# Kernel tuning notes

Hardware: AMD Instinct MI355X
Metric: run time of the kernel (lower is better)

Reference implementation:

```python
import jax, jax.numpy as jnp
import numpy as np

N = 100000   # nodes
E = 800000   # edges
G = 64       # graphs in batch
H_LSTM = 256


def setup_inputs() -> dict:
    key = jax.random.key(0)
    ks = jax.random.split(key, 24)

    def rn(k, shape, scale=0.05):
        return jax.random.normal(k, shape, dtype=jnp.float32) * scale

    inp = {
        "x": jax.random.normal(ks[0], (N, 32), dtype=jnp.float32),
        "edge_index": jax.random.randint(ks[1], (2, E), 0, N, dtype=jnp.int64),
        "batch_idx": jnp.sort(jax.random.randint(ks[2], (N,), 0, G, dtype=jnp.int64)),
        # GCN layer weights (in_dim x out_dim) + bias
        "W1": rn(ks[3], (32, 128)),   "b1": jnp.zeros((128,), jnp.float32),
        "W2": rn(ks[4], (128, 256)),  "b2": jnp.zeros((256,), jnp.float32),
        "W3": rn(ks[5], (256, 512)),  "b3": jnp.zeros((512,), jnp.float32),
        # LSTM layer 0: input 512 -> hidden 256, gates order (i,f,g,o)
        "Wih0": rn(ks[6], (4 * H_LSTM, 512)), "Whh0": rn(ks[7], (4 * H_LSTM, H_LSTM)),
        "bih0": jnp.zeros((4 * H_LSTM,), jnp.float32), "bhh0": jnp.zeros((4 * H_LSTM,), jnp.float32),
        # LSTM layer 1: input 256 -> hidden 256
        "Wih1": rn(ks[8], (4 * H_LSTM, H_LSTM)), "Whh1": rn(ks[9], (4 * H_LSTM, H_LSTM)),
        "bih1": jnp.zeros((4 * H_LSTM,), jnp.float32), "bhh1": jnp.zeros((4 * H_LSTM,), jnp.float32),
        # output projection 256 -> 512
        "Wp": rn(ks[10], (512, H_LSTM)), "bp": jnp.zeros((512,), jnp.float32),
    }
    return inp


def _lstm_cell(xt, Wih, Whh, bih, bhh):
    B = xt.shape[0]
    H = Whh.shape[1]
    h0 = jnp.zeros((B, H), xt.dtype)
    c0 = jnp.zeros((B, H), xt.dtype)
    gates = xt @ Wih.T + h0 @ Whh.T + bih + bhh  # [B, 4H]
    i = jax.nn.sigmoid(gates[:, 0 * H:1 * H])
    f = jax.nn.sigmoid(gates[:, 1 * H:2 * H])
    g = jnp.tanh(gates[:, 2 * H:3 * H])
    o = jax.nn.sigmoid(gates[:, 3 * H:4 * H])
    c = f * c0 + i * g
    return o * jnp.tanh(c)


def reference(x, edge_index, batch_idx, W1, b1, W2, b2, W3, b3,
              Wih0, Whh0, bih0, bhh0, Wih1, Whh1, bih1, bhh1, Wp, bp):
    src, dst = edge_index[0], edge_index[1]
    # symmetric GCN normalization with self-loops (PyG GCNConv default)
    deg = jax.ops.segment_sum(jnp.ones((E,), x.dtype), dst, num_segments=N) + 1.0
    dinv = jax.lax.rsqrt(deg)
    edge_norm = (dinv[src] * dinv[dst])[:, None]
    self_norm = (dinv * dinv)[:, None]

    def gcn(h, W, b):
        h = h @ W                                            # transform first (smaller gather)
        msg = h[src] * edge_norm                             # [E, out]
        agg = jax.ops.segment_sum(msg, dst, num_segments=N)  # scatter-add to targets
        agg = agg + h * self_norm                            # self-loop contribution
        return jax.nn.relu(agg + b)

    h = gcn(x, W1, b1)
    h = gcn(h, W2, b2)
    h = gcn(h, W3, b3)  # [N, 512]

    # global mean pool per graph
    counts = jax.ops.segment_sum(jnp.ones((N,), h.dtype), batch_idx, num_segments=G)
    pooled = jax.ops.segment_sum(h, batch_idx, num_segments=G) / jnp.maximum(counts, 1.0)[:, None]

    # 2-layer LSTM over seq_len=1 (zero initial state)
    h1 = _lstm_cell(pooled, Wih0, Whh0, bih0, bhh0)
    h2 = _lstm_cell(h1, Wih1, Whh1, bih1, bhh1)
    return h2 @ Wp.T + bp  # [G, 512]
```

## Files before the change

kernel.cpp:

```cpp
#include <hip/hip_runtime.h>
#include <math.h>
#include <type_traits>


__device__ __forceinline__ float bf2f(unsigned short u) {
    union { unsigned int i; float f; } v; v.i = ((unsigned int)u) << 16; return v.f;
}
__device__ __forceinline__ unsigned short f2bf(float f) {
    union { float f_; unsigned int i; } v; v.f_ = f;
    unsigned int x = v.i;
    return (unsigned short)((x + 0x7fffu + ((x >> 16) & 1u)) >> 16);
}
__device__ __forceinline__ float sigm(float x) { return 1.f / (1.f + expf(-x)); }

typedef __attribute__((ext_vector_type(8))) short short8;
typedef __attribute__((ext_vector_type(16))) float f32x16;

__device__ __forceinline__ void nt_store8(unsigned short* p, ushort4 o) {
    unsigned long long ob;
    __builtin_memcpy(&ob, &o, 8);
    __builtin_nontemporal_store(ob, (unsigned long long*)p);
}


__global__ void k_init(int* __restrict__ indeg, int* __restrict__ cursor,
                       int* __restrict__ gstart, int* __restrict__ gend,
                       float* __restrict__ pooled, int N) {
    int i = blockIdx.x * 256 + threadIdx.x;
    if (i < N) indeg[i] = 0;
    else if (i < 2 * N) cursor[i - N] = 0;
    else if (i < 2 * N + 64) gstart[i - 2 * N] = 0;
    else if (i < 2 * N + 128) gend[i - 2 * N - 64] = 0;
    else if (i < 2 * N + 128 + 64 * 512) pooled[i - 2 * N - 128] = 0.f;
}


template <int K, int NC>
__device__ __forceinline__ void prep_elem(const float* __restrict__ W,
                                          unsigned short* __restrict__ Wf, int idx) {
    constexpr int S = K / 16;
    int lane = idx & 63;
    int ts = idx >> 6;
    int s = ts % S, t = ts / S;
    int n = t * 32 + (lane & 31);
    int kb = s * 16 + (lane >> 5) * 8;
    short8 o;
    #pragma unroll
    for (int j = 0; j < 8; ++j) o[j] = (short)f2bf(W[(size_t)(kb + j) * NC + n]);
    *(short8*)(Wf + (size_t)idx * 8) = o;
}

__global__ void k_count(const int* __restrict__ dst, int* __restrict__ indeg, int E,
                        const float* __restrict__ W1, unsigned short* __restrict__ Wf1,
                        const float* __restrict__ W2, unsigned short* __restrict__ Wf2,
                        const float* __restrict__ W3, unsigned short* __restrict__ Wf3) {
    constexpr int P1 = 32 * 128 / 8, P2 = 128 * 256 / 8, P3 = 256 * 512 / 8;
    int i = blockIdx.x * 256 + threadIdx.x;
    if (i < E) atomicAdd(&indeg[dst[i]], 1);
    if (i < P1) prep_elem<32, 128>(W1, Wf1, i);
    else if (i < P1 + P2) prep_elem<128, 256>(W2, Wf2, i - P1);
    else if (i < P1 + P2 + P3) prep_elem<256, 512>(W3, Wf3, i - P1 - P2);
}


__global__ __launch_bounds__(1024) void k_scan1(const int* __restrict__ in, int* __restrict__ out,
                                                int* __restrict__ bsum, float* __restrict__ dinv,
                                                const float* __restrict__ x,
                                                unsigned short* __restrict__ xs,
                                                int N) {
    __shared__ int sd[1024];
    __shared__ float sdv[1024];
    int tid = threadIdx.x;
    int i = blockIdx.x * 1024 + tid;
    int v = (i < N) ? in[i] : 0;
    float dv = rsqrtf((float)v + 1.0f);
    if (i < N) dinv[i] = dv;
    sdv[tid] = dv;
    sd[tid] = v;
    __syncthreads();
    for (int s = 1; s < 1024; s <<= 1) {
        int t = (tid >= s) ? sd[tid - s] : 0;
        __syncthreads();
        sd[tid] += t;
        __syncthreads();
    }
    if (i < N) out[i] = sd[tid] - v;
    if (tid == 1023) bsum[blockIdx.x] = sd[1023];
    int base = blockIdx.x * 1024;
    const float4* x4 = (const float4*)x;
    ushort4* xs4 = (ushort4*)xs;
    #pragma unroll
    for (int rep = 0; rep < 8; ++rep) {
        int j = rep * 1024 + tid;
        int node = base + (j >> 3);
        if (node < N) {
            float4 t = x4[(size_t)base * 8 + j];
            float s = sdv[j >> 3];
            ushort4 o;
            o.x = f2bf(t.x * s); o.y = f2bf(t.y * s);
            o.z = f2bf(t.z * s); o.w = f2bf(t.w * s);
            xs4[(size_t)base * 8 + j] = o;
        }
    }
}

__global__ __launch_bounds__(256) void k_scan2(int* __restrict__ bsum, int nb) {
    __shared__ int sd[256];
    int tid = threadIdx.x;
    int v = (tid < nb) ? bsum[tid] : 0;
    sd[tid] = v;
    __syncthreads();
    for (int s = 1; s < 256; s <<= 1) {
        int t = (tid >= s) ? sd[tid - s] : 0;
        __syncthreads();
        sd[tid] += t;
        __syncthreads();
    }
    if (tid < nb) bsum[tid] = sd[tid] - v;
    if (tid == 0) bsum[nb] = sd[255];
}

__global__ __launch_bounds__(1024) void k_scan3(int* __restrict__ off, const int* __restrict__ bsum,
                                                const int* __restrict__ batch,
                                                int* __restrict__ gstart, int* __restrict__ gend,
                                                int N, int nb) {
    int i = blockIdx.x * 1024 + threadIdx.x;
    if (i < N) {
        off[i] += bsum[i >> 10];
        int g = batch[i];
        if (i == 0 || batch[i - 1] != g) gstart[g] = i;
        if (i == N - 1 || batch[i + 1] != g) gend[g] = i + 1;
    } else if (i == N) {
        off[N] = bsum[nb];
    }
}

__global__ void k_fill(const int* __restrict__ src, const int* __restrict__ dst,
                       const int* __restrict__ off, int* __restrict__ cursor,
                       int* __restrict__ csrc, int E) {
    int i = blockIdx.x * 256 + threadIdx.x;
    if (i >= E) return;
    int d = dst[i];
    int p = off[d] + atomicAdd(&cursor[d], 1);
    csrc[p] = src[i];
}


__global__ __launch_bounds__(256) void k_aggL1(
        const unsigned short* __restrict__ Hin, const float* __restrict__ dinv,
        const int* __restrict__ off, const int* __restrict__ csrc,
        unsigned short* __restrict__ out, int N) {
    constexpr int F = 32;
    int wv = __builtin_amdgcn_readfirstlane(
        (int)((blockIdx.x * 256u + threadIdx.x) >> 6));
    if (wv >= N) return;
    int lane = threadIdx.x & 63;
    int grp = lane >> 3;
    int cl = (lane & 7) * 4;
    int s0 = off[wv], s1 = off[wv + 1];
    int L = s1 - s0;
    float corr = 1.0f - (float)(((L + 7) & ~7) - L);
    float dn = dinv[wv];
    float acc[4] = {0.f, 0.f, 0.f, 0.f};
    for (int e = s0; e < s1; e += 8) {
        int ee = e + grp;
        int ix = csrc[ee];
        int idx = (ee < s1) ? ix : wv;
        ushort4 v = *(const ushort4*)(Hin + (size_t)idx * F + cl);
        acc[0] += bf2f(v.x); acc[1] += bf2f(v.y);
        acc[2] += bf2f(v.z); acc[3] += bf2f(v.w);
    }
    #pragma unroll
    for (int msk = 8; msk <= 32; msk <<= 1) {
        acc[0] += __shfl_xor(acc[0], msk, 64);
        acc[1] += __shfl_xor(acc[1], msk, 64);
        acc[2] += __shfl_xor(acc[2], msk, 64);
        acc[3] += __shfl_xor(acc[3], msk, 64);
    }
    if (grp == 0) {
        ushort4 sv = *(const ushort4*)(Hin + (size_t)wv * F + cl);
        ushort4 o;
        o.x = f2bf((acc[0] + corr * bf2f(sv.x)) * dn);
        o.y = f2bf((acc[1] + corr * bf2f(sv.y)) * dn);
        o.z = f2bf((acc[2] + corr * bf2f(sv.z)) * dn);
        o.w = f2bf((acc[3] + corr * bf2f(sv.w)) * dn);
        nt_store8(out + (size_t)wv * F + cl, o);
    }
}

__global__ __launch_bounds__(256) void k_aggL2(
        const unsigned short* __restrict__ Hin, const float* __restrict__ dinv,
        const int* __restrict__ off, const int* __restrict__ csrc,
        unsigned short* __restrict__ out, int N) {
    constexpr int F = 128;
    int wv = __builtin_amdgcn_readfirstlane(
        (int)((blockIdx.x * 256u + threadIdx.x) >> 6));
    if (wv >= N) return;
    int lane = threadIdx.x & 63;
    int half = lane >> 5;
    int fb = (lane & 31) * 4;
    int s0 = off[wv], s1 = off[wv + 1];
    int L = s1 - s0;
    float corrTot = 1.0f - (float)(((L + 15) & ~15) - L);
    float acc[4] = {0.f, 0.f, 0.f, 0.f};

    for (int e = s0; e < s1; e += 16) {
        int idx[8];
        #pragma unroll
        for (int j = 0; j < 8; ++j) {
            int ee = e + j * 2 + half;
            int ix = csrc[ee];
            idx[j] = (ee < s1) ? ix : wv;
        }
        ushort4 d0[8];
        #pragma unroll
        for (int j = 0; j < 8; ++j)
            d0[j] = *(const ushort4*)(Hin + (size_t)idx[j] * F + fb);
        #pragma unroll
        for (int j = 0; j < 8; ++j) {
            acc[0] += bf2f(d0[j].x); acc[1] += bf2f(d0[j].y);
            acc[2] += bf2f(d0[j].z); acc[3] += bf2f(d0[j].w);
        }
    }
    #pragma unroll
    for (int k = 0; k < 4; ++k) acc[k] += __shfl_xor(acc[k], 32, 64);

    if (half == 0) {
        float dn = dinv[wv];
        ushort4 sv = *(const ushort4*)(Hin + (size_t)wv * F + fb);
        ushort4 o;
        o.x = f2bf((acc[0] + corrTot * bf2f(sv.x)) * dn);
        o.y = f2bf((acc[1] + corrTot * bf2f(sv.y)) * dn);
        o.z = f2bf((acc[2] + corrTot * bf2f(sv.z)) * dn);
        o.w = f2bf((acc[3] + corrTot * bf2f(sv.w)) * dn);
        nt_store8(out + (size_t)wv * F + fb, o);
    }
}

__global__ __launch_bounds__(256) void k_aggL3pair(
        const unsigned short* __restrict__ Hin, const float* __restrict__ dinv,
        const int* __restrict__ off, const int* __restrict__ csrc,
        unsigned short* __restrict__ out, int N) {
    constexpr int F = 256;
    int wv = __builtin_amdgcn_readfirstlane(
        (int)((blockIdx.x * 256u + threadIdx.x) >> 6));
    if (wv >= N) return;
    int lane = threadIdx.x & 63;
    int half = lane >> 5;
    int fb = (lane & 31) * 8;
    int s0 = off[wv], s1 = off[wv + 1];
    int L = s1 - s0;
    float corrTot = 1.0f - (float)(((L + 15) & ~15) - L);
    float acc[8];
    #pragma unroll
    for (int k = 0; k < 8; ++k) acc[k] = 0.f;

    for (int e = s0; e < s1; e += 16) {
        int idx[8];
        #pragma unroll
        for (int j = 0; j < 8; ++j) {
            int ee = e + j * 2 + half;
            int ix = csrc[ee];
            idx[j] = (ee < s1) ? ix : wv;
        }
        short8 d0[8];
        #pragma unroll
        for (int j = 0; j < 8; ++j)
            d0[j] = *(const short8*)(Hin + (size_t)idx[j] * F + fb);
        #pragma unroll
        for (int j = 0; j < 8; ++j) {
            #pragma unroll
            for (int k = 0; k < 8; ++k)
                acc[k] += bf2f((unsigned short)d0[j][k]);
        }
    }
    #pragma unroll
    for (int k = 0; k < 8; ++k) acc[k] += __shfl_xor(acc[k], 32, 64);

    if (half == 0) {
        float dn = dinv[wv];
        short8 selfv = *(const short8*)(Hin + (size_t)wv * F + fb);
        short8 o;
        #pragma unroll
        for (int k = 0; k < 8; ++k)
            o[k] = (short)f2bf((acc[k] + corrTot * bf2f((unsigned short)selfv[k])) * dn);
        __builtin_nontemporal_store(o, (short8*)(out + (size_t)wv * F + fb));
    }
}


template <int K, int NC, int POOL>
__device__ __forceinline__ void gemm_body(
        const unsigned short* __restrict__ A, const unsigned short* __restrict__ Wf,
        const float* __restrict__ bias, const float* __restrict__ dinv,
        unsigned short* __restrict__ C,
        float* __restrict__ pooled, float* __restrict__ partial,
        int* __restrict__ gtile, const int* __restrict__ batch, int M) {
    constexpr int S = K / 16;
    constexpr int CPR = K / 8;
    constexpr int NT = NC / 32;
    __shared__ unsigned short sA[64 * K];
    __shared__ int sbat[POOL ? 64 : 1];
    __shared__ float sdv[POOL ? 1 : 64];
    int tid = threadIdx.x, lane = tid & 63, w = tid >> 6;
    int q = lane >> 5, m = lane & 31;
    int row0 = blockIdx.x * 64;

    if (tid < 64) {
        int rr = row0 + tid; if (rr > M - 1) rr = M - 1;
        if (POOL) sbat[tid] = batch[rr];
        else      sdv[tid] = dinv[rr];
    }

    #pragma unroll
    for (int i = 0; i < (64 * CPR) / 256; ++i) {
        int g = i * 256 + tid;
        int mm = g / CPR, kc = g % CPR;
        int grow = row0 + mm; if (grow > M - 1) grow = M - 1;
        short8 v = *(const short8*)(A + (size_t)grow * K + kc * 8);
        int xm = (CPR >= 8) ? (mm & 7) : ((mm >> 1) & 3);
        *(short8*)(sA + (size_t)(mm * CPR + (kc ^ xm)) * 8) = v;
    }
    __syncthreads();

    int gmin = 0; bool fast = false;
    unsigned int selMask = 0;
    if (POOL) {
        gmin = sbat[0];
        fast = (sbat[63] - gmin) <= 1;
        if (tid == 0) gtile[blockIdx.x] = gmin;
        #pragma unroll
        for (int half = 0; half < 2; ++half) {
            #pragma unroll
            for (int j = 0; j < 16; ++j) {
                int rloc = half * 32 + (j & 3) + 8 * (j >> 2) + 4 * q;
                if (sbat[rloc] != gmin) selMask |= 1u << (half * 16 + j);
            }
        }
    }

    const short8* Wf8 = (const short8*)Wf;
    for (int t = w; t < NT; t += 4) {
        short8 bF[S];
        #pragma unroll
        for (int s = 0; s < S; ++s) bF[s] = Wf8[(t * S + s) * 64 + lane];
        int colBase = t * 32 + m;
        float bv = bias[colBase];
        float p0 = 0.f, p1 = 0.f;
        #pragma unroll
        for (int half = 0; half < 2; ++half) {
            int mrow = half * 32 + m;
            int xm = (CPR >= 8) ? (mrow & 7) : ((mrow >> 1) & 3);
            f32x16 acc;
            #pragma unroll
            for (int j = 0; j < 16; ++j) acc[j] = 0.f;
            #pragma unroll
            for (int s = 0; s < S; ++s) {
                int kc = s * 2 + q;
                short8 aF = *(const short8*)(sA + (size_t)(mrow * CPR + (kc ^ xm)) * 8);
                acc = __builtin_amdgcn_mfma_f32_32x32x16_bf16(aF, bF[s], acc, 0, 0, 0);
            }
            #pragma unroll
            for (int j = 0; j < 16; ++j) {
                int rloc = half * 32 + (j & 3) + 8 * (j >> 2) + 4 * q;
                int row = row0 + rloc;
                if (row < M) {
                    float v = fmaxf(acc[j] + bv, 0.f);
                    if (POOL) {
                        if (fast) {
                            bool sel = (selMask >> (half * 16 + j)) & 1u;
                            p0 += sel ? 0.f : v;
                            p1 += sel ? v : 0.f;
                        } else {
                            atomicAdd(&pooled[(size_t)sbat[rloc] * NC + colBase], v);
                        }
                    } else {
                        C[(size_t)row * NC + colBase] = f2bf(v * sdv[rloc]);
                    }
                }
            }
        }
        if (POOL) {
            p0 += __shfl_xor(p0, 32, 64);
            p1 += __shfl_xor(p1, 32, 64);
            if (q == 0) {
                partial[((size_t)blockIdx.x * 2 + 0) * NC + colBase] = p0;
                partial[((size_t)blockIdx.x * 2 + 1) * NC + colBase] = p1;
            }
        }
    }
}

__global__ __launch_bounds__(256, 2) void k_gemmL1(
        const unsigned short* __restrict__ A, const unsigned short* __restrict__ Wf,
        const float* __restrict__ bias, const float* __restrict__ dinv,
        unsigned short* __restrict__ C, int M) {
    gemm_body<32, 128, 0>(A, Wf, bias, dinv, C, nullptr, nullptr, nullptr, nullptr, M);
}

__global__ __launch_bounds__(256, 2) void k_gemmL2(
        const unsigned short* __restrict__ A, const unsigned short* __restrict__ Wf,
        const float* __restrict__ bias, const float* __restrict__ dinv,
        unsigned short* __restrict__ C, int M) {
    gemm_body<128, 256, 0>(A, Wf, bias, dinv, C, nullptr, nullptr, nullptr, nullptr, M);
}

__global__ __launch_bounds__(256, 2) void k_gemmL3pool(
        const unsigned short* __restrict__ A, const unsigned short* __restrict__ Wf,
        const float* __restrict__ bias, float* __restrict__ pooled,
        float* __restrict__ partial, int* __restrict__ gtile,
        const int* __restrict__ batch, int M) {
    gemm_body<256, 512, 1>(A, Wf, bias, nullptr, nullptr, pooled, partial, gtile, batch, M);
}


__global__ __launch_bounds__(256) void k_pool(
        const float* __restrict__ pooled, const float* __restrict__ partial,
        const int* __restrict__ gtile,
        const int* __restrict__ gstart, const int* __restrict__ gend,
        float* __restrict__ xmean) {
    int g = blockIdx.x, tid = threadIdx.x;
    int gs = gstart[g], ge = gend[g];
    float inv = 1.f / fmaxf((float)(ge - gs), 1.f);
    float a0 = pooled[g * 512 + tid];
    float a1 = pooled[g * 512 + 256 + tid];
    if (ge > gs) {
        int t0 = gs >> 6, t1 = (ge - 1) >> 6;
        for (int t = t0; t <= t1; ++t) {
            unsigned int slot = (unsigned int)(g - gtile[t]);
            if (slot < 2u) {
                const float* p = partial + ((size_t)t * 2 + slot) * 512;
                a0 += p[tid];
                a1 += p[tid + 256];
            }
        }
    }
    xmean[g * 512 + tid]       = a0 * inv;
    xmean[g * 512 + 256 + tid] = a1 * inv;
}

__device__ __forceinline__ float dot8(const float* __restrict__ w,
                                      float4 x0, float4 x1) {
    float4 a = *(const float4*)w, b = *(const float4*)(w + 4);
    return a.x * x0.x + a.y * x0.y + a.z * x0.z + a.w * x0.w +
           b.x * x1.x + b.y * x1.y + b.z * x1.z + b.w * x1.w;
}
__device__ __forceinline__ float dot4(const float* __restrict__ w, float4 x) {
    float4 a = *(const float4*)w;
    return a.x * x.x + a.y * x.y + a.z * x.z + a.w * x.w;
}

__global__ __launch_bounds__(256) void k_lstm0(
        const float* __restrict__ xmean, const float* __restrict__ Wih0,
        const float* __restrict__ bih0, const float* __restrict__ bhh0,
        float* __restrict__ h1) {
    int wid = (int)((blockIdx.x * 256u + threadIdx.x) >> 6);
    int lane = threadIdx.x & 63;
    int g = wid >> 8, hu = wid & 255;
    int k0 = lane * 8;
    const float* xp = xmean + g * 512 + k0;
    float4 x0 = *(const float4*)xp, x1 = *(const float4*)(xp + 4);
    float ai = dot8(Wih0 + (size_t)hu * 512 + k0, x0, x1);
    float ag = dot8(Wih0 + (size_t)(hu + 512) * 512 + k0, x0, x1);
    float ao = dot8(Wih0 + (size_t)(hu + 768) * 512 + k0, x0, x1);
    #pragma unroll
    for (int msk = 32; msk >= 1; msk >>= 1) {
        ai += __shfl_xor(ai, msk, 64);
        ag += __shfl_xor(ag, msk, 64);
        ao += __shfl_xor(ao, msk, 64);
    }
    if (lane == 0) {
        ai += bih0[hu]       + bhh0[hu];
        ag += bih0[hu + 512] + bhh0[hu + 512];
        ao += bih0[hu + 768] + bhh0[hu + 768];
        float c0 = sigm(ai) * tanhf(ag);
        h1[g * 256 + hu] = sigm(ao) * tanhf(c0);
    }
}

__global__ __launch_bounds__(256) void k_lstm1(
        const float* __restrict__ h1, const float* __restrict__ Wih1,
        const float* __restrict__ bih1, const float* __restrict__ bhh1,
        float* __restrict__ h2) {
    int wid = (int)((blockIdx.x * 256u + threadIdx.x) >> 6);
    int lane = threadIdx.x & 63;
    int g = wid >> 8, hu = wid & 255;
    int k0 = lane * 4;
    float4 x = *(const float4*)(h1 + g * 256 + k0);
    float ai = dot4(Wih1 + (size_t)hu * 256 + k0, x);
    float ag = dot4(Wih1 + (size_t)(hu + 512) * 256 + k0, x);
    float ao = dot4(Wih1 + (size_t)(hu + 768) * 256 + k0, x);
    #pragma unroll
    for (int msk = 32; msk >= 1; msk >>= 1) {
        ai += __shfl_xor(ai, msk, 64);
        ag += __shfl_xor(ag, msk, 64);
        ao += __shfl_xor(ao, msk, 64);
    }
    if (lane == 0) {
        ai += bih1[hu]       + bhh1[hu];
        ag += bih1[hu + 512] + bhh1[hu + 512];
        ao += bih1[hu + 768] + bhh1[hu + 768];
        float c1 = sigm(ai) * tanhf(ag);
        h2[g * 256 + hu] = sigm(ao) * tanhf(c1);
    }
}

__global__ __launch_bounds__(256) void k_out(
        const float* __restrict__ h2, const float* __restrict__ Wp,
        const float* __restrict__ bp, float* __restrict__ out) {
    int wid = (int)((blockIdx.x * 256u + threadIdx.x) >> 6);
    int lane = threadIdx.x & 63;
    int g = wid >> 9, r = wid & 511;
    int k0 = lane * 4;
    float4 x = *(const float4*)(h2 + g * 256 + k0);
    float a = dot4(Wp + (size_t)r * 256 + k0, x);
    #pragma unroll
    for (int msk = 32; msk >= 1; msk >>= 1) a += __shfl_xor(a, msk, 64);
    if (lane == 0) out[g * 512 + r] = a + bp[r];
}


extern "C" void kernel_launch(void* const* d_in, const int* in_sizes, int n_in,
                              void* d_out, int out_size, void* d_ws, size_t ws_size,
                              hipStream_t stream) {
    const float* x     = (const float*)d_in[0];
    const int*   eidx  = (const int*)d_in[1];
    const int*   batch = (const int*)d_in[2];
    const float* W1 = (const float*)d_in[3];  const float* b1 = (const float*)d_in[4];
    const float* W2 = (const float*)d_in[5];  const float* b2 = (const float*)d_in[6];
    const float* W3 = (const float*)d_in[7];  const float* b3 = (const float*)d_in[8];
    const float* Wih0 = (const float*)d_in[9];
    const float* bih0 = (const float*)d_in[11];
    const float* bhh0 = (const float*)d_in[12];
    const float* Wih1 = (const float*)d_in[13];
    const float* bih1 = (const float*)d_in[15];
    const float* bhh1 = (const float*)d_in[16];
    const float* Wp = (const float*)d_in[17]; const float* bp = (const float*)d_in[18];
    float* out = (float*)d_out;

    const int N = in_sizes[0] / 32;
    const int E = in_sizes[1] / 2;
    const int* src = eidx;
    const int* dst = eidx + E;
    const int rowTiles = (N + 63) / 64;

    char* w = (char*)d_ws;
    auto alloc = [&](size_t bytes) {
        char* p = w;
        w += (bytes + 255) & ~(size_t)255;
        return p;
    };
    unsigned short* buf1 = (unsigned short*)alloc((size_t)N * 256 * 2);
    unsigned short* buf2 = (unsigned short*)alloc((size_t)N * 256 * 2);
    unsigned short* Wf1  = (unsigned short*)alloc(128 * 32 * 2);
    unsigned short* Wf2  = (unsigned short*)alloc(256 * 128 * 2);
    unsigned short* Wf3  = (unsigned short*)alloc(512 * 256 * 2);
    int*   indeg  = (int*)alloc((size_t)N * 4);
    int*   off    = (int*)alloc((size_t)(N + 1) * 4);
    int*   cursor = (int*)alloc((size_t)N * 4);
    float* dinv   = (float*)alloc((size_t)N * 4);
    int*   csrc   = (int*)alloc((size_t)(E + 64) * 4);
    unsigned short* xs = (unsigned short*)alloc((size_t)N * 32 * 2 + 65536);
    int*   bsum   = (int*)alloc(8192);
    int*   gstart = (int*)alloc(64 * 4);
    int*   gend   = (int*)alloc(64 * 4);
    float* pooled = (float*)alloc(64 * 512 * 4);
    float* xmean  = (float*)alloc(64 * 512 * 4);
    float* h1buf  = (float*)alloc(64 * 256 * 4);
    float* h2buf  = (float*)alloc(64 * 256 * 4);

    float* partial = (float*)xs;
    int*   gtile   = cursor;

    int initTot = 2 * N + 128 + 64 * 512;
    k_init<<<(initTot + 255) / 256, 256, 0, stream>>>(indeg, cursor, gstart, gend, pooled, N);
    k_count<<<(E + 255) / 256, 256, 0, stream>>>(dst, indeg, E, W1, Wf1, W2, Wf2, W3, Wf3);
    int nb = (N + 1023) / 1024;
    k_scan1<<<nb, 1024, 0, stream>>>(indeg, off, bsum, dinv, x, xs, N);
    k_scan2<<<1, 256, 0, stream>>>(bsum, nb);
    k_scan3<<<(N + 1 + 1023) / 1024, 1024, 0, stream>>>(off, bsum, batch, gstart, gend, N, nb);
    k_fill<<<(E + 255) / 256, 256, 0, stream>>>(src, dst, off, cursor, csrc, E);

    int aggBlocks = (N + 3) / 4;

    k_aggL1<<<aggBlocks, 256, 0, stream>>>(xs, dinv, off, csrc, buf1, N);
    k_gemmL1<<<rowTiles, 256, 0, stream>>>(buf1, Wf1, b1, dinv, buf2, N);
    k_aggL2<<<aggBlocks, 256, 0, stream>>>(buf2, dinv, off, csrc, buf1, N);
    k_gemmL2<<<rowTiles, 256, 0, stream>>>(buf1, Wf2, b2, dinv, buf2, N);
    k_aggL3pair<<<aggBlocks, 256, 0, stream>>>(buf2, dinv, off, csrc, buf1, N);
    k_gemmL3pool<<<rowTiles, 256, 0, stream>>>(buf1, Wf3, b3, pooled, partial, gtile, batch, N);

    k_pool<<<64, 256, 0, stream>>>(pooled, partial, gtile, gstart, gend, xmean);
    k_lstm0<<<4096, 256, 0, stream>>>(xmean, Wih0, bih0, bhh0, h1buf);
    k_lstm1<<<4096, 256, 0, stream>>>(h1buf, Wih1, bih1, bhh1, h2buf);
    k_out<<<8192, 256, 0, stream>>>(h2buf, Wp, bp, out);
}
```

Before: 447.2 us.

## Fuse layer-1 GEMM into aggregation kernel and fold block-sum scan into scan3

Folds the small 32x128 layer-1 transform into the layer-1 aggregation kernel: each wave aggregates one node's 32 features, stages the row in shared memory, and computes 128 outputs with FP32 FMAs against W1 loaded into LDS. This drops the layer-1 GEMM kernel, its weight pre-conversion and one round trip of the intermediate buffer. It also removes the single-block k_scan2 launch by having every k_scan3 block reduce the block sums itself. The trade-off is that every aggregation block reloads the 16KB W1 into LDS, which adds load traffic and LDS pressure, and k_scan3 does redundant reductions across all blocks.

```diff
diff --git a/kernel.cpp b/kernel.cpp
--- a/kernel.cpp
+++ b/kernel.cpp
@@ -51,15 +51,13 @@
 }
 
 __global__ void k_count(const int* __restrict__ dst, int* __restrict__ indeg, int E,
-                        const float* __restrict__ W1, unsigned short* __restrict__ Wf1,
                         const float* __restrict__ W2, unsigned short* __restrict__ Wf2,
                         const float* __restrict__ W3, unsigned short* __restrict__ Wf3) {
-    constexpr int P1 = 32 * 128 / 8, P2 = 128 * 256 / 8, P3 = 256 * 512 / 8;
+    constexpr int P2 = 128 * 256 / 8, P3 = 256 * 512 / 8;
     int i = blockIdx.x * 256 + threadIdx.x;
     if (i < E) atomicAdd(&indeg[dst[i]], 1);
-    if (i < P1) prep_elem<32, 128>(W1, Wf1, i);
-    else if (i < P1 + P2) prep_elem<128, 256>(W2, Wf2, i - P1);
-    else if (i < P1 + P2 + P3) prep_elem<256, 512>(W3, Wf3, i - P1 - P2);
+    if (i < P2) prep_elem<128, 256>(W2, Wf2, i);
+    else if (i < P2 + P3) prep_elem<256, 512>(W3, Wf3, i - P2);
 }
 
 
@@ -104,34 +102,34 @@
     }
 }
 
-__global__ __launch_bounds__(256) void k_scan2(int* __restrict__ bsum, int nb) {
-    __shared__ int sd[256];
-    int tid = threadIdx.x;
-    int v = (tid < nb) ? bsum[tid] : 0;
-    sd[tid] = v;
-    __syncthreads();
-    for (int s = 1; s < 256; s <<= 1) {
-        int t = (tid >= s) ? sd[tid - s] : 0;
-        __syncthreads();
-        sd[tid] += t;
-        __syncthreads();
-    }
-    if (tid < nb) bsum[tid] = sd[tid] - v;
-    if (tid == 0) bsum[nb] = sd[255];
-}
-
 __global__ __launch_bounds__(1024) void k_scan3(int* __restrict__ off, const int* __restrict__ bsum,
                                                 const int* __restrict__ batch,
                                                 int* __restrict__ gstart, int* __restrict__ gend,
                                                 int N, int nb) {
-    int i = blockIdx.x * 1024 + threadIdx.x;
+    __shared__ int red[32];
+    int tid = threadIdx.x, lane = tid & 63, wid = tid >> 6;
+    int bid = blockIdx.x;
+    int v  = (tid < nb) ? bsum[tid] : 0;
+    int vb = (tid < bid) ? v : 0;
+    #pragma unroll
+    for (int msk = 1; msk <= 32; msk <<= 1) {
+        v  += __shfl_xor(v,  msk, 64);
+        vb += __shfl_xor(vb, msk, 64);
+    }
+    if (lane == 0) { red[wid * 2] = v; red[wid * 2 + 1] = vb; }
+    __syncthreads();
+    int sAll = 0, sBefore = 0;
+    #pragma unroll
+    for (int u = 0; u < 16; ++u) { sAll += red[u * 2]; sBefore += red[u * 2 + 1]; }
+
+    int i = bid * 1024 + tid;
     if (i < N) {
-        off[i] += bsum[i >> 10];
+        off[i] += sBefore;
         int g = batch[i];
         if (i == 0 || batch[i - 1] != g) gstart[g] = i;
         if (i == N - 1 || batch[i + 1] != g) gend[g] = i + 1;
     } else if (i == N) {
-        off[N] = bsum[nb];
+        off[N] = sAll;
     }
 }
 
@@ -146,15 +144,27 @@
 }
 
 
-__global__ __launch_bounds__(256) void k_aggL1(
-        const unsigned short* __restrict__ Hin, const float* __restrict__ dinv,
+__global__ __launch_bounds__(256) void k_aggL1f(
+        const unsigned short* __restrict__ Hin,
+        const float* __restrict__ dinv,
         const int* __restrict__ off, const int* __restrict__ csrc,
+        const float* __restrict__ W1, const float* __restrict__ b1,
         unsigned short* __restrict__ out, int N) {
     constexpr int F = 32;
-    int wv = __builtin_amdgcn_readfirstlane(
-        (int)((blockIdx.x * 256u + threadIdx.x) >> 6));
+    __shared__ float sW[32 * 128];
+    __shared__ float srow[4][32];
+    int tid = threadIdx.x;
+    #pragma unroll
+    for (int i = 0; i < 4; ++i) {
+        int j = i * 1024 + tid * 4;
+        *(float4*)&sW[j] = *(const float4*)&W1[j];
+    }
+    __syncthreads();
+
+    int w = tid >> 6;
+    int wv = (int)((blockIdx.x * 256u + tid) >> 6);
     if (wv >= N) return;
-    int lane = threadIdx.x & 63;
+    int lane = tid & 63;
     int grp = lane >> 3;
     int cl = (lane & 7) * 4;
     int s0 = off[wv], s1 = off[wv + 1];
@@ -177,16 +187,30 @@
         acc[2] += __shfl_xor(acc[2], msk, 64);
         acc[3] += __shfl_xor(acc[3], msk, 64);
     }
-    if (grp == 0) {
-        ushort4 sv = *(const ushort4*)(Hin + (size_t)wv * F + cl);
-        ushort4 o;
-        o.x = f2bf((acc[0] + corr * bf2f(sv.x)) * dn);
-        o.y = f2bf((acc[1] + corr * bf2f(sv.y)) * dn);
-        o.z = f2bf((acc[2] + corr * bf2f(sv.z)) * dn);
-        o.w = f2bf((acc[3] + corr * bf2f(sv.w)) * dn);
-        nt_store8(out + (size_t)wv * F + cl, o);
-    }
-}
+    ushort4 sv = *(const ushort4*)(Hin + (size_t)wv * F + cl);
+    if (lane < 8) {
+        float4 a;
+        a.x = (acc[0] + corr * bf2f(sv.x)) * dn;
+        a.y = (acc[1] + corr * bf2f(sv.y)) * dn;
+        a.z = (acc[2] + corr * bf2f(sv.z)) * dn;
+        a.w = (acc[3] + corr * bf2f(sv.w)) * dn;
+        *(float4*)&srow[w][cl] = a;
+    }
+    float2 bv = *(const float2*)&b1[2 * lane];
+    float c0 = bv.x, c1 = bv.y;
+    #pragma unroll
+    for (int k = 0; k < 32; ++k) {
+        float ak = srow[w][k];
+        float2 wk = *(const float2*)&sW[k * 128 + 2 * lane];
+        c0 = fmaf(ak, wk.x, c0);
+        c1 = fmaf(ak, wk.y, c1);
+    }
+    c0 = fmaxf(c0, 0.f) * dn;
+    c1 = fmaxf(c1, 0.f) * dn;
+    ushort2 o; o.x = f2bf(c0); o.y = f2bf(c1);
+    *(ushort2*)(out + (size_t)wv * 128 + 2 * lane) = o;
+}
+
 
 __global__ __launch_bounds__(256) void k_aggL2(
         const unsigned short* __restrict__ Hin, const float* __restrict__ dinv,
@@ -391,13 +415,6 @@
     }
 }
 
-__global__ __launch_bounds__(256, 2) void k_gemmL1(
-        const unsigned short* __restrict__ A, const unsigned short* __restrict__ Wf,
-        const float* __restrict__ bias, const float* __restrict__ dinv,
-        unsigned short* __restrict__ C, int M) {
-    gemm_body<32, 128, 0>(A, Wf, bias, dinv, C, nullptr, nullptr, nullptr, nullptr, M);
-}
-
 __global__ __launch_bounds__(256, 2) void k_gemmL2(
         const unsigned short* __restrict__ A, const unsigned short* __restrict__ Wf,
         const float* __restrict__ bias, const float* __restrict__ dinv,
@@ -552,7 +569,6 @@
     };
     unsigned short* buf1 = (unsigned short*)alloc((size_t)N * 256 * 2);
     unsigned short* buf2 = (unsigned short*)alloc((size_t)N * 256 * 2);
-    unsigned short* Wf1  = (unsigned short*)alloc(128 * 32 * 2);
     unsigned short* Wf2  = (unsigned short*)alloc(256 * 128 * 2);
     unsigned short* Wf3  = (unsigned short*)alloc(512 * 256 * 2);
     int*   indeg  = (int*)alloc((size_t)N * 4);
@@ -574,17 +590,15 @@
 
     int initTot = 2 * N + 128 + 64 * 512;
     k_init<<<(initTot + 255) / 256, 256, 0, stream>>>(indeg, cursor, gstart, gend, pooled, N);
-    k_count<<<(E + 255) / 256, 256, 0, stream>>>(dst, indeg, E, W1, Wf1, W2, Wf2, W3, Wf3);
+    k_count<<<(E + 255) / 256, 256, 0, stream>>>(dst, indeg, E, W2, Wf2, W3, Wf3);
     int nb = (N + 1023) / 1024;
     k_scan1<<<nb, 1024, 0, stream>>>(indeg, off, bsum, dinv, x, xs, N);
-    k_scan2<<<1, 256, 0, stream>>>(bsum, nb);
     k_scan3<<<(N + 1 + 1023) / 1024, 1024, 0, stream>>>(off, bsum, batch, gstart, gend, N, nb);
     k_fill<<<(E + 255) / 256, 256, 0, stream>>>(src, dst, off, cursor, csrc, E);
 
     int aggBlocks = (N + 3) / 4;
 
-    k_aggL1<<<aggBlocks, 256, 0, stream>>>(xs, dinv, off, csrc, buf1, N);
-    k_gemmL1<<<rowTiles, 256, 0, stream>>>(buf1, Wf1, b1, dinv, buf2, N);
+    k_aggL1f<<<aggBlocks, 256, 0, stream>>>(xs, dinv, off, csrc, W1, b1, buf2, N);
     k_aggL2<<<aggBlocks, 256, 0, stream>>>(buf2, dinv, off, csrc, buf1, N);
     k_gemmL2<<<rowTiles, 256, 0, stream>>>(buf1, Wf2, b2, dinv, buf2, N);
     k_aggL3pair<<<aggBlocks, 256, 0, stream>>>(buf2, dinv, off, csrc, buf1, N);
```

Measured after the change: 458.8 us. 1.03x slower.
